# Kernel tuning notes

Measured on AMD Instinct MI355X. Metric: run time of the kernel, lower is better.

The kernel has to match this reference:

```python
import jax, jax.numpy as jnp
import numpy as np

BS, NINP, NHID, K, T = 2048, 512, 512, 16, 8
M = NHID // K  # per-block hidden = 32
ATT_D = 16     # read/write key dim
TAU = 0.5


def setup_inputs() -> dict:
    key = jax.random.key(0)
    ks = jax.random.split(key, 10)
    s = 0.1
    return {
        "x": jax.random.normal(ks[0], (BS, NINP), jnp.float32),
        "h": jax.random.normal(ks[1], (BS, NHID), jnp.float32),
        # stacked GRUCell params across templates (torch gate order: r, z, n)
        "W_ih": jax.random.normal(ks[2], (T, 3 * M, NINP), jnp.float32) * s,
        "W_hh": jax.random.normal(ks[3], (T, 3 * M, M), jnp.float32) * s,
        "b_ih": jax.random.normal(ks[4], (T, 3 * M), jnp.float32) * s,
        "b_hh": jax.random.normal(ks[5], (T, 3 * M), jnp.float32) * s,
        # GroupLinearLayer weights (no bias): read has 1 group, write has T groups
        "w_read": jax.random.normal(ks[6], (1, M, ATT_D), jnp.float32) * s,
        "w_write": jax.random.normal(ks[7], (T, M, ATT_D), jnp.float32) * s,
        # pre-sampled Gumbel noise for gumbel_softmax, shape [bs*k, T]
        "gumbel_noise": jax.random.gumbel(ks[8], (BS * K, T), jnp.float32),
    }


def reference(x, h, W_ih, W_hh, b_ih, b_hh, w_read, w_write, gumbel_noise):
    bs = h.shape[0]
    N = bs * K
    # blockify hidden: [bs, nhid] -> [N, m]
    h2 = h.reshape(N, M)
    # tile input across blocks: [bs, ninp] -> [N, ninp]
    xin = jnp.broadcast_to(x[:, None, :], (bs, K, NINP)).reshape(N, NINP)
    # read key: GroupLinearLayer with 1 group -> [N, ATT_D]
    h_read = h2 @ w_read[0]
    # all-template GRUCell as two grouped GEMMs: [T, N, 3m]
    gi = jnp.einsum('ni,tgi->tng', xin, W_ih) + b_ih[:, None, :]
    gh = jnp.einsum('nm,tgm->tng', h2, W_hh) + b_hh[:, None, :]
    r = jax.nn.sigmoid(gi[..., :M] + gh[..., :M])
    z = jax.nn.sigmoid(gi[..., M:2 * M] + gh[..., M:2 * M])
    n = jnp.tanh(gi[..., 2 * M:] + r * gh[..., 2 * M:])
    hnext = (1.0 - z) * n + z * h2[None]            # [T, N, m]
    hnext = hnext.transpose(1, 0, 2)                # [N, T, m]
    # write keys: grouped linear per template -> [N, T, ATT_D]
    write_key = jnp.einsum('ntm,tmf->ntf', hnext, w_write)
    # attention logits: bmm(h_read[N,1,f], write_key^T) -> [N, T]
    logits = jnp.einsum('nf,ntf->nt', h_read, write_key)
    # hard gumbel-softmax (tau=0.5) with straight-through estimator
    y_soft = jax.nn.softmax((logits + gumbel_noise) / TAU, axis=-1)
    y_hard = jax.nn.one_hot(jnp.argmax(y_soft, axis=-1), T, dtype=y_soft.dtype)
    att = y_hard + y_soft - jax.lax.stop_gradient(y_soft)  # [N, T]
    # combine templates (bmm with [N,1,T] then mean over singleton dim)
    h_out = jnp.einsum('nt,ntm->nm', att, hnext)    # [N, m]
    h_out = h_out.reshape(bs, K * M)
    att_out = jax.lax.stop_gradient(att).reshape(bs, K, T)
    return h_out, att_out
```

## Files before the change

### kernel.cpp

```cpp
#include <hip/hip_runtime.h>

#define NB_BS   2048
#define NB_NINP 512
#define NB_NHID 512
#define NB_K    16
#define NB_T    8
#define NB_M    32
#define NB_C    768
#define H_OUT_ELEMS (NB_BS * NB_NHID)

__global__ __launch_bounds__(1024)
void k1_gemm_gi(const float* __restrict__ x, const float* __restrict__ Wih,
                const float* __restrict__ bih, const float* __restrict__ bhh,
                float* __restrict__ gi)
{
    __shared__ __align__(16) float As[2][32][68];
    __shared__ __align__(16) float Bs[2][32][100];
    __shared__ float ACCX[512][13];

    const int tid  = threadIdx.x;
    const int kg   = tid >> 9;
    const int ttid = tid & 511;
    const int row0 = blockIdx.x * 64;
    const int col0 = blockIdx.y * 96;
    const int rg   = ttid >> 5;
    const int cg   = ttid & 31;
    const int kb0  = kg * 256;

    const int ar = ttid >> 3, akq = (ttid & 7) * 4;
    const int bc0 = ttid >> 3,        bkq0 = (ttid & 7) * 4;
    const int bc1 = 64 + (ttid >> 3), bkq1 = (ttid & 7) * 4;

    float4 a0 = *(const float4*)&x[(size_t)(row0 + ar) * NB_NINP + kb0 + akq];
    float4 b0 = *(const float4*)&Wih[(size_t)(col0 + bc0) * NB_NINP + kb0 + bkq0];
    float4 b1;
    if (ttid < 256)
        b1 = *(const float4*)&Wih[(size_t)(col0 + bc1) * NB_NINP + kb0 + bkq1];

    float acc[4][3];
    #pragma unroll
    for (int i = 0; i < 4; ++i)
        #pragma unroll
        for (int e = 0; e < 3; ++e) acc[i][e] = 0.f;

    for (int slab = 0; slab < 8; ++slab) {
        __syncthreads();
        As[kg][akq+0][ar]=a0.x; As[kg][akq+1][ar]=a0.y;
        As[kg][akq+2][ar]=a0.z; As[kg][akq+3][ar]=a0.w;
        Bs[kg][bkq0+0][bc0]=b0.x; Bs[kg][bkq0+1][bc0]=b0.y;
        Bs[kg][bkq0+2][bc0]=b0.z; Bs[kg][bkq0+3][bc0]=b0.w;
        if (ttid < 256) {
            Bs[kg][bkq1+0][bc1]=b1.x; Bs[kg][bkq1+1][bc1]=b1.y;
            Bs[kg][bkq1+2][bc1]=b1.z; Bs[kg][bkq1+3][bc1]=b1.w;
        }
        __syncthreads();
        if (slab < 7) {
            const int kb = kb0 + (slab + 1) * 32;
            a0 = *(const float4*)&x[(size_t)(row0 + ar) * NB_NINP + kb + akq];
            b0 = *(const float4*)&Wih[(size_t)(col0 + bc0) * NB_NINP + kb + bkq0];
            if (ttid < 256)
                b1 = *(const float4*)&Wih[(size_t)(col0 + bc1) * NB_NINP + kb + bkq1];
        }
        #pragma unroll
        for (int kk = 0; kk < 32; ++kk) {
            const float4 av = *(const float4*)&As[kg][kk][rg * 4];
            const float w0 = Bs[kg][kk][cg];
            const float w1 = Bs[kg][kk][cg + 32];
            const float w2 = Bs[kg][kk][cg + 64];
            const float avv[4] = {av.x, av.y, av.z, av.w};
            #pragma unroll
            for (int i = 0; i < 4; ++i) {
                acc[i][0] = fmaf(avv[i], w0, acc[i][0]);
                acc[i][1] = fmaf(avv[i], w1, acc[i][1]);
                acc[i][2] = fmaf(avv[i], w2, acc[i][2]);
            }
        }
    }

    __syncthreads();
    if (kg == 1) {
        #pragma unroll
        for (int i = 0; i < 4; ++i)
            #pragma unroll
            for (int e = 0; e < 3; ++e) ACCX[ttid][i * 3 + e] = acc[i][e];
    }
    __syncthreads();
    if (kg == 0) {
        float bias[3];
        #pragma unroll
        for (int e = 0; e < 3; ++e) {
            const int c = col0 + cg + e * 32;
            bias[e] = bih[c] + (e < 2 ? bhh[c] : 0.f);
        }
        #pragma unroll
        for (int i = 0; i < 4; ++i) {
            const size_t base = (size_t)(row0 + rg * 4 + i) * NB_C + col0 + cg;
            #pragma unroll
            for (int e = 0; e < 3; ++e)
                gi[base + e * 32] = acc[i][e] + ACCX[ttid][i * 3 + e] + bias[e];
        }
    }
}

__global__ __launch_bounds__(1024)
__attribute__((amdgpu_waves_per_eu(4, 4)))
void k2_fused(const float* __restrict__ h,      const float* __restrict__ Whh,
              const float* __restrict__ bhh,    const float* __restrict__ wread,
              const float* __restrict__ wwrite, const float* __restrict__ gumb,
              const float* __restrict__ gi,     float* __restrict__ out)
{
    __shared__ __align__(16) float4 P[3][32][64];
    __shared__ __align__(16) float4 WWT4[16][64];
    __shared__ __align__(16) float WR[512];
    __shared__ __align__(16) float HT[8][32][20];
    __shared__ __align__(16) float HR2T[8][16][20];

    const int tid  = threadIdx.x;
    const int wave = tid >> 6, lane = tid & 63;
    const int bl   = wave >> 1, kh = wave & 1;
    const int b    = blockIdx.x * 8 + bl;
    const int m_   = lane & 31, half = lane >> 5;

    float* PF = (float*)P;
    for (int i = tid; i < 24576; i += 1024) {
        const int c = i >> 5, mm = i & 31;
        const int t = c / 96, rem = c - t * 96;
        const int gc = rem >> 5, mout = rem & 31;
        const int j  = (t >> 1) * 3 + gc;
        const int sl = ((t & 1) * 32 + mout) ^ (mm & 7);
        PF[(((j >> 2) * 32 + mm) * 64 + sl) * 4 + (j & 3)] = Whh[i];
    }
    for (int i = tid; i < 4096; i += 1024) {
        const int t = i >> 9, mo = (i >> 4) & 31, f = i & 15;
        ((float*)WWT4)[(f * 64 + (t & 1) * 32 + mo) * 4 + (t >> 1)] = wwrite[i];
    }
    if (tid < 512) WR[tid] = wread[tid];
    #pragma unroll
    for (int e = 0; e < 4; ++e) {
        const int idx = kh * 256 + e * 64 + lane;
        HT[bl][idx & 31][idx >> 5] = h[(size_t)b * NB_NHID + idx];
    }
    __syncthreads();

    {
        const int kq = kh * 8 + (lane >> 3);
        const int f0 = (lane & 7) * 2;
        float s0 = 0.f, s1 = 0.f;
        #pragma unroll 8
        for (int mm = 0; mm < 32; ++mm) {
            const float hv = HT[bl][mm][kq];
            s0 = fmaf(hv, WR[mm * 16 + f0], s0);
            s1 = fmaf(hv, WR[mm * 16 + f0 + 1], s1);
        }
        HR2T[bl][f0    ][kq] = s0;
        HR2T[bl][f0 + 1][kq] = s1;
    }

    float gi_r[4][3], bhn[4];
    #pragma unroll
    for (int p = 0; p < 4; ++p) {
        const int t = 2 * p + half;
        #pragma unroll
        for (int gc = 0; gc < 3; ++gc)
            gi_r[p][gc] = gi[(size_t)b * NB_C + t * 96 + gc * 32 + m_];
        bhn[p] = bhh[t * 96 + 64 + m_];
    }

    #pragma unroll 1
    for (int pass = 0; pass < 2; ++pass) {
        const int k0 = kh * 8 + pass * 4;

        float acc[4][12];
        #pragma unroll
        for (int r = 0; r < 4; ++r)
            #pragma unroll
            for (int j = 0; j < 12; ++j) acc[r][j] = 0.f;

        #pragma unroll 4
        for (int mm = 0; mm < 32; ++mm) {
            const int sw = lane ^ (mm & 7);
            const float4 w0 = P[0][mm][sw];
            const float4 w1 = P[1][mm][sw];
            const float4 w2 = P[2][mm][sw];
            const float4 hv = *(const float4*)&HT[bl][mm][k0];
            const float wj[12] = {w0.x,w0.y,w0.z,w0.w, w1.x,w1.y,w1.z,w1.w,
                                  w2.x,w2.y,w2.z,w2.w};
            const float hr4[4] = {hv.x, hv.y, hv.z, hv.w};
            #pragma unroll
            for (int r = 0; r < 4; ++r)
                #pragma unroll
                for (int j = 0; j < 12; ++j)
                    acc[r][j] = fmaf(hr4[r], wj[j], acc[r][j]);
        }

        float ww[4][4];
        #pragma unroll
        for (int r = 0; r < 4; ++r)
            #pragma unroll
            for (int p = 0; p < 4; ++p) ww[r][p] = 0.f;
        #pragma unroll 4
        for (int f = 0; f < 16; ++f) {
            const float4 wt4 = WWT4[f][half * 32 + m_];
            const float4 hka = *(const float4*)&HR2T[bl][f][k0];
            const float wt[4] = {wt4.x, wt4.y, wt4.z, wt4.w};
            const float hk[4] = {hka.x, hka.y, hka.z, hka.w};
            #pragma unroll
            for (int r = 0; r < 4; ++r)
                #pragma unroll
                for (int p = 0; p < 4; ++p)
                    ww[r][p] = fmaf(hk[r], wt[p], ww[r][p]);
        }

        #pragma unroll
        for (int r = 0; r < 4; ++r) {
            const int k = k0 + r;
            const float h2v = HT[bl][m_][k];
            float hn[4], lg[4];
            #pragma unroll
            for (int p = 0; p < 4; ++p) {
                const float xr = gi_r[p][0] + acc[r][p*3+0];
                const float xz = gi_r[p][1] + acc[r][p*3+1];
                const float gn = bhn[p]     + acc[r][p*3+2];
                const float rg = 1.f / (1.f + __expf(-xr));
                const float zg = 1.f / (1.f + __expf(-xz));
                const float xn = gi_r[p][2] + rg * gn;
                const float e2 = __expf(2.f * xn);
                const float tn = 1.f - 2.f / (e2 + 1.f);
                const float hv2 = (1.f - zg) * tn + zg * h2v;
                hn[p] = hv2;
                float part = hv2 * ww[r][p];
                part += __shfl_xor(part, 1, 64);
                part += __shfl_xor(part, 2, 64);
                part += __shfl_xor(part, 4, 64);
                part += __shfl_xor(part, 8, 64);
                part += __shfl_xor(part, 16, 64);
                lg[p] = part;
            }
            float s[8];
            #pragma unroll
            for (int p = 0; p < 4; ++p) {
                const float oth = __shfl_xor(lg[p], 32, 64);
                s[2*p]   = half ? oth   : lg[p];
                s[2*p+1] = half ? lg[p] : oth;
            }
            const float* gp = gumb + ((size_t)b * NB_K + k) * NB_T;
            const float4 ga = *(const float4*)gp;
            const float4 gb = *(const float4*)(gp + 4);
            const float gv[8] = {ga.x,ga.y,ga.z,ga.w, gb.x,gb.y,gb.z,gb.w};
            float best = s[0] + gv[0]; int bt = 0;
            #pragma unroll
            for (int t2 = 1; t2 < 8; ++t2) {
                const float v = s[t2] + gv[t2];
                if (v > best) { best = v; bt = t2; }
            }
            const int pstar = bt >> 1, hstar = bt & 1;
            float hsel = hn[0];
            hsel = (pstar == 1) ? hn[1] : hsel;
            hsel = (pstar == 2) ? hn[2] : hsel;
            hsel = (pstar == 3) ? hn[3] : hsel;
            if (half == hstar)
                out[(size_t)b * NB_NHID + k * 32 + m_] = hsel;
            if (lane < 8)
                out[H_OUT_ELEMS + ((size_t)b * NB_K + k) * NB_T + lane] =
                    (lane == bt) ? 1.f : 0.f;
        }
    }
}

extern "C" void kernel_launch(void* const* d_in, const int* in_sizes, int n_in,
                              void* d_out, int out_size, void* d_ws, size_t ws_size,
                              hipStream_t stream) {
    const float* x      = (const float*)d_in[0];
    const float* h      = (const float*)d_in[1];
    const float* Wih    = (const float*)d_in[2];
    const float* Whh    = (const float*)d_in[3];
    const float* bih    = (const float*)d_in[4];
    const float* bhh    = (const float*)d_in[5];
    const float* wread  = (const float*)d_in[6];
    const float* wwrite = (const float*)d_in[7];
    const float* gumb   = (const float*)d_in[8];
    float* out = (float*)d_out;
    float* gi  = (float*)d_ws;

    k1_gemm_gi<<<dim3(32, 8), 1024, 0, stream>>>(x, Wih, bih, bhh, gi);
    k2_fused<<<dim3(256), 1024, 0, stream>>>(h, Whh, bhh, wread, wwrite,
                                             gumb, gi, out);
}
```

Baseline: 87.47 us.

## Retile gi GEMM to 512 threads, transpose-reduce logits, prioritize GEMM waves

The input-projection GEMM kernel now runs 512 threads per block, each computing a 4x6 output tile with float2 shared loads and float2 stores. This raises per-thread register reuse and cuts LDS traffic, but each block has half as many threads. In the fused kernel, the per-template logit butterfly reductions become a transposed reduction that merges partial sums across templates and exchanges the results through a small shared array, cutting the shuffle count. It also raises wave priority around the hidden-state GEMM loop. The shared-memory exchange relies on wave-synchronous behaviour with no explicit barrier, which is a correctness risk.

```diff
diff --git a/kernel.cpp b/kernel.cpp
--- a/kernel.cpp
+++ b/kernel.cpp
@@ -9,71 +9,73 @@
 #define NB_C    768
 #define H_OUT_ELEMS (NB_BS * NB_NHID)
 
-__global__ __launch_bounds__(1024)
+__global__ __launch_bounds__(512, 2)
 void k1_gemm_gi(const float* __restrict__ x, const float* __restrict__ Wih,
                 const float* __restrict__ bih, const float* __restrict__ bhh,
                 float* __restrict__ gi)
 {
     __shared__ __align__(16) float As[2][32][68];
     __shared__ __align__(16) float Bs[2][32][100];
-    __shared__ float ACCX[512][13];
+    __shared__ float ACCX[256][25];
 
     const int tid  = threadIdx.x;
-    const int kg   = tid >> 9;
-    const int ttid = tid & 511;
+    const int kg   = tid >> 8;
+    const int ttid = tid & 255;
     const int row0 = blockIdx.x * 64;
     const int col0 = blockIdx.y * 96;
-    const int rg   = ttid >> 5;
-    const int cg   = ttid & 31;
+    const int rg   = ttid >> 4;
+    const int cg   = ttid & 15;
     const int kb0  = kg * 256;
 
-    const int ar = ttid >> 3, akq = (ttid & 7) * 4;
-    const int bc0 = ttid >> 3,        bkq0 = (ttid & 7) * 4;
-    const int bc1 = 64 + (ttid >> 3), bkq1 = (ttid & 7) * 4;
-
-    float4 a0 = *(const float4*)&x[(size_t)(row0 + ar) * NB_NINP + kb0 + akq];
-    float4 b0 = *(const float4*)&Wih[(size_t)(col0 + bc0) * NB_NINP + kb0 + bkq0];
-    float4 b1;
-    if (ttid < 256)
-        b1 = *(const float4*)&Wih[(size_t)(col0 + bc1) * NB_NINP + kb0 + bkq1];
-
-    float acc[4][3];
+    const int ar0 = ttid >> 3, akq = (ttid & 7) * 4, ar1 = ar0 + 32;
+    const int c0 = ttid >> 3, c1 = c0 + 32, c2 = c0 + 64;
+
+    float4 a0 = *(const float4*)&x[(size_t)(row0 + ar0) * NB_NINP + kb0 + akq];
+    float4 a1 = *(const float4*)&x[(size_t)(row0 + ar1) * NB_NINP + kb0 + akq];
+    float4 b0 = *(const float4*)&Wih[(size_t)(col0 + c0) * NB_NINP + kb0 + akq];
+    float4 b1 = *(const float4*)&Wih[(size_t)(col0 + c1) * NB_NINP + kb0 + akq];
+    float4 b2 = *(const float4*)&Wih[(size_t)(col0 + c2) * NB_NINP + kb0 + akq];
+
+    float acc[4][6];
     #pragma unroll
     for (int i = 0; i < 4; ++i)
         #pragma unroll
-        for (int e = 0; e < 3; ++e) acc[i][e] = 0.f;
+        for (int e = 0; e < 6; ++e) acc[i][e] = 0.f;
 
     for (int slab = 0; slab < 8; ++slab) {
         __syncthreads();
-        As[kg][akq+0][ar]=a0.x; As[kg][akq+1][ar]=a0.y;
-        As[kg][akq+2][ar]=a0.z; As[kg][akq+3][ar]=a0.w;
-        Bs[kg][bkq0+0][bc0]=b0.x; Bs[kg][bkq0+1][bc0]=b0.y;
-        Bs[kg][bkq0+2][bc0]=b0.z; Bs[kg][bkq0+3][bc0]=b0.w;
-        if (ttid < 256) {
-            Bs[kg][bkq1+0][bc1]=b1.x; Bs[kg][bkq1+1][bc1]=b1.y;
-            Bs[kg][bkq1+2][bc1]=b1.z; Bs[kg][bkq1+3][bc1]=b1.w;
-        }
+        As[kg][akq+0][ar0]=a0.x; As[kg][akq+1][ar0]=a0.y;
+        As[kg][akq+2][ar0]=a0.z; As[kg][akq+3][ar0]=a0.w;
+        As[kg][akq+0][ar1]=a1.x; As[kg][akq+1][ar1]=a1.y;
+        As[kg][akq+2][ar1]=a1.z; As[kg][akq+3][ar1]=a1.w;
+        Bs[kg][akq+0][c0]=b0.x; Bs[kg][akq+1][c0]=b0.y;
+        Bs[kg][akq+2][c0]=b0.z; Bs[kg][akq+3][c0]=b0.w;
+        Bs[kg][akq+0][c1]=b1.x; Bs[kg][akq+1][c1]=b1.y;
+        Bs[kg][akq+2][c1]=b1.z; Bs[kg][akq+3][c1]=b1.w;
+        Bs[kg][akq+0][c2]=b2.x; Bs[kg][akq+1][c2]=b2.y;
+        Bs[kg][akq+2][c2]=b2.z; Bs[kg][akq+3][c2]=b2.w;
         __syncthreads();
         if (slab < 7) {
             const int kb = kb0 + (slab + 1) * 32;
-            a0 = *(const float4*)&x[(size_t)(row0 + ar) * NB_NINP + kb + akq];
-            b0 = *(const float4*)&Wih[(size_t)(col0 + bc0) * NB_NINP + kb + bkq0];
-            if (ttid < 256)
-                b1 = *(const float4*)&Wih[(size_t)(col0 + bc1) * NB_NINP + kb + bkq1];
+            a0 = *(const float4*)&x[(size_t)(row0 + ar0) * NB_NINP + kb + akq];
+            a1 = *(const float4*)&x[(size_t)(row0 + ar1) * NB_NINP + kb + akq];
+            b0 = *(const float4*)&Wih[(size_t)(col0 + c0) * NB_NINP + kb + akq];
+            b1 = *(const float4*)&Wih[(size_t)(col0 + c1) * NB_NINP + kb + akq];
+            b2 = *(const float4*)&Wih[(size_t)(col0 + c2) * NB_NINP + kb + akq];
         }
         #pragma unroll
         for (int kk = 0; kk < 32; ++kk) {
             const float4 av = *(const float4*)&As[kg][kk][rg * 4];
-            const float w0 = Bs[kg][kk][cg];
-            const float w1 = Bs[kg][kk][cg + 32];
-            const float w2 = Bs[kg][kk][cg + 64];
+            const float2 w0 = *(const float2*)&Bs[kg][kk][cg * 6];
+            const float2 w1 = *(const float2*)&Bs[kg][kk][cg * 6 + 2];
+            const float2 w2 = *(const float2*)&Bs[kg][kk][cg * 6 + 4];
             const float avv[4] = {av.x, av.y, av.z, av.w};
-            #pragma unroll
-            for (int i = 0; i < 4; ++i) {
-                acc[i][0] = fmaf(avv[i], w0, acc[i][0]);
-                acc[i][1] = fmaf(avv[i], w1, acc[i][1]);
-                acc[i][2] = fmaf(avv[i], w2, acc[i][2]);
-            }
+            const float wvv[6] = {w0.x, w0.y, w1.x, w1.y, w2.x, w2.y};
+            #pragma unroll
+            for (int i = 0; i < 4; ++i)
+                #pragma unroll
+                for (int e = 0; e < 6; ++e)
+                    acc[i][e] = fmaf(avv[i], wvv[e], acc[i][e]);
         }
     }
 
@@ -82,22 +84,27 @@
         #pragma unroll
         for (int i = 0; i < 4; ++i)
             #pragma unroll
-            for (int e = 0; e < 3; ++e) ACCX[ttid][i * 3 + e] = acc[i][e];
+            for (int e = 0; e < 6; ++e) ACCX[ttid][i * 6 + e] = acc[i][e];
     }
     __syncthreads();
     if (kg == 0) {
-        float bias[3];
-        #pragma unroll
-        for (int e = 0; e < 3; ++e) {
-            const int c = col0 + cg + e * 32;
-            bias[e] = bih[c] + (e < 2 ? bhh[c] : 0.f);
+        float bias[6];
+        #pragma unroll
+        for (int e = 0; e < 6; ++e) {
+            const int cl = cg * 6 + e;
+            const int c  = col0 + cl;
+            bias[e] = bih[c] + (cl < 64 ? bhh[c] : 0.f);
         }
         #pragma unroll
         for (int i = 0; i < 4; ++i) {
-            const size_t base = (size_t)(row0 + rg * 4 + i) * NB_C + col0 + cg;
-            #pragma unroll
-            for (int e = 0; e < 3; ++e)
-                gi[base + e * 32] = acc[i][e] + ACCX[ttid][i * 3 + e] + bias[e];
+            const size_t base = (size_t)(row0 + rg * 4 + i) * NB_C + col0 + cg * 6;
+            #pragma unroll
+            for (int e = 0; e < 6; e += 2) {
+                float2 o;
+                o.x = acc[i][e]   + ACCX[ttid][i*6+e]   + bias[e];
+                o.y = acc[i][e+1] + ACCX[ttid][i*6+e+1] + bias[e+1];
+                *(float2*)&gi[base + e] = o;
+            }
         }
     }
 }
@@ -114,6 +121,7 @@
     __shared__ __align__(16) float WR[512];
     __shared__ __align__(16) float HT[8][32][20];
     __shared__ __align__(16) float HR2T[8][16][20];
+    __shared__ __align__(16) float LG[8][16][8];
 
     const int tid  = threadIdx.x;
     const int wave = tid >> 6, lane = tid & 63;
@@ -176,6 +184,7 @@
             #pragma unroll
             for (int j = 0; j < 12; ++j) acc[r][j] = 0.f;
 
+        __builtin_amdgcn_s_setprio(1);
         #pragma unroll 4
         for (int mm = 0; mm < 32; ++mm) {
             const int sw = lane ^ (mm & 7);
@@ -192,6 +201,7 @@
                 for (int j = 0; j < 12; ++j)
                     acc[r][j] = fmaf(hr4[r], wj[j], acc[r][j]);
         }
+        __builtin_amdgcn_s_setprio(0);
 
         float ww[4][4];
         #pragma unroll
@@ -215,7 +225,7 @@
         for (int r = 0; r < 4; ++r) {
             const int k = k0 + r;
             const float h2v = HT[bl][m_][k];
-            float hn[4], lg[4];
+            float hn[4], part[4];
             #pragma unroll
             for (int p = 0; p < 4; ++p) {
                 const float xr = gi_r[p][0] + acc[r][p*3+0];
@@ -228,31 +238,35 @@
                 const float tn = 1.f - 2.f / (e2 + 1.f);
                 const float hv2 = (1.f - zg) * tn + zg * h2v;
                 hn[p] = hv2;
-                float part = hv2 * ww[r][p];
-                part += __shfl_xor(part, 1, 64);
-                part += __shfl_xor(part, 2, 64);
-                part += __shfl_xor(part, 4, 64);
-                part += __shfl_xor(part, 8, 64);
-                part += __shfl_xor(part, 16, 64);
-                lg[p] = part;
+                part[p] = hv2 * ww[r][p];
             }
-            float s[8];
-            #pragma unroll
-            for (int p = 0; p < 4; ++p) {
-                const float oth = __shfl_xor(lg[p], 32, 64);
-                s[2*p]   = half ? oth   : lg[p];
-                s[2*p+1] = half ? lg[p] : oth;
+            #pragma unroll
+            for (int p = 0; p < 4; ++p)
+                part[p] += __shfl_xor(part[p], 16, 64);
+            const bool b4 = (lane & 16) != 0, b3 = (lane & 8) != 0;
+            float v01 = b4 ? part[1] : part[0];
+            float v23 = b4 ? part[3] : part[2];
+            v01 += __shfl_xor(v01, 8, 64);
+            v23 += __shfl_xor(v23, 8, 64);
+            float v = b3 ? v23 : v01;
+            v += __shfl_xor(v, 4, 64);
+            v += __shfl_xor(v, 2, 64);
+            v += __shfl_xor(v, 1, 64);
+            if ((lane & 7) == 0) {
+                const int p_ = ((lane >> 4) & 1) | (((lane >> 3) & 1) << 1);
+                LG[bl][k][2 * p_ + half] = v;
             }
+            const float4 l0 = *(const float4*)&LG[bl][k][0];
+            const float4 l1 = *(const float4*)&LG[bl][k][4];
             const float* gp = gumb + ((size_t)b * NB_K + k) * NB_T;
             const float4 ga = *(const float4*)gp;
             const float4 gb = *(const float4*)(gp + 4);
-            const float gv[8] = {ga.x,ga.y,ga.z,ga.w, gb.x,gb.y,gb.z,gb.w};
-            float best = s[0] + gv[0]; int bt = 0;
-            #pragma unroll
-            for (int t2 = 1; t2 < 8; ++t2) {
-                const float v = s[t2] + gv[t2];
-                if (v > best) { best = v; bt = t2; }
-            }
+            const float s[8] = {l0.x+ga.x, l0.y+ga.y, l0.z+ga.z, l0.w+ga.w,
+                                l1.x+gb.x, l1.y+gb.y, l1.z+gb.z, l1.w+gb.w};
+            float best = s[0]; int bt = 0;
+            #pragma unroll
+            for (int t2 = 1; t2 < 8; ++t2)
+                if (s[t2] > best) { best = s[t2]; bt = t2; }
             const int pstar = bt >> 1, hstar = bt & 1;
             float hsel = hn[0];
             hsel = (pstar == 1) ? hn[1] : hsel;
@@ -282,7 +296,7 @@
     float* out = (float*)d_out;
     float* gi  = (float*)d_ws;
 
-    k1_gemm_gi<<<dim3(32, 8), 1024, 0, stream>>>(x, Wih, bih, bhh, gi);
+    k1_gemm_gi<<<dim3(32, 8), 512, 0, stream>>>(x, Wih, bih, bhh, gi);
     k2_fused<<<dim3(256), 1024, 0, stream>>>(h, Whh, bhh, wread, wwrite,
                                              gumb, gi, out);
 }
```

Result: faster. 80.92 us (-7.5%).
